# Kernel optimization log

Measured on AMD Instinct MI355X. Metric: run time of the kernel, lower is better.

Reference implementation:

```python
import jax, jax.numpy as jnp
import numpy as np

N, F_IN, E, DIM, G, C = 50000, 128, 800000, 64, 128, 10
BN_EPS = 1e-5


def setup_inputs() -> dict:
    key = jax.random.key(0)
    ks = jax.random.split(key, 24)
    x = jax.random.normal(ks[0], (N, F_IN), dtype=jnp.float32)
    edge_index = jax.random.randint(ks[1], (2, E), 0, N, dtype=jnp.int32)
    batch = jnp.sort(jax.random.randint(ks[2], (N,), 0, G, dtype=jnp.int32))

    def lin(k, fan_in, shape):
        b = 1.0 / np.sqrt(fan_in)
        return jax.random.uniform(k, shape, jnp.float32, -b, b)

    # layer 1 MLP: [F_IN->DIM], [DIM->DIM]
    W1a, b1a = lin(ks[3], F_IN, (F_IN, DIM)), lin(ks[4], F_IN, (DIM,))
    W1b, b1b = lin(ks[5], DIM, (DIM, DIM)), lin(ks[6], DIM, (DIM,))
    # layers 2-5 MLPs stacked: [4, DIM, DIM]
    Wa = jnp.stack([lin(jax.random.fold_in(ks[7], i), DIM, (DIM, DIM)) for i in range(4)])
    ba = jnp.stack([lin(jax.random.fold_in(ks[8], i), DIM, (DIM,)) for i in range(4)])
    Wb = jnp.stack([lin(jax.random.fold_in(ks[9], i), DIM, (DIM, DIM)) for i in range(4)])
    bb = jnp.stack([lin(jax.random.fold_in(ks[10], i), DIM, (DIM,)) for i in range(4)])
    gammas = jnp.ones((5, DIM), jnp.float32)
    betas = jnp.zeros((5, DIM), jnp.float32)
    fc1_w, fc1_b = lin(ks[11], DIM, (DIM, DIM)), lin(ks[12], DIM, (DIM,))
    fc2_w, fc2_b = lin(ks[13], DIM, (DIM, C)), lin(ks[14], DIM, (C,))
    return dict(x=x, edge_index=edge_index, batch=batch,
                W1a=W1a, b1a=b1a, W1b=W1b, b1b=b1b,
                Wa=Wa, ba=ba, Wb=Wb, bb=bb,
                gammas=gammas, betas=betas,
                fc1_w=fc1_w, fc1_b=fc1_b, fc2_w=fc2_w, fc2_b=fc2_b)


def _gin_conv(x, edge_index, W1, b1, W2, b2):
    # PyG GINConv (eps=0): MLP((1+eps)*x + scatter_add of source feats at targets)
    agg = jax.ops.segment_sum(x[edge_index[0]], edge_index[1], num_segments=N)
    h = x + agg
    h = jnp.maximum(h @ W1 + b1, 0.0) @ W2 + b2
    return h


def _bn(h, gamma, beta):
    # BatchNorm1d, training mode (batch statistics, biased variance)
    mean = h.mean(axis=0)
    var = h.var(axis=0)
    return (h - mean) * jax.lax.rsqrt(var + BN_EPS) * gamma + beta


def reference(x, edge_index, batch, W1a, b1a, W1b, b1b, Wa, ba, Wb, bb,
              gammas, betas, fc1_w, fc1_b, fc2_w, fc2_b):
    h = jnp.maximum(_gin_conv(x, edge_index, W1a, b1a, W1b, b1b), 0.0)
    h = _bn(h, gammas[0], betas[0])
    for i in range(4):
        h = jnp.maximum(_gin_conv(h, edge_index, Wa[i], ba[i], Wb[i], bb[i]), 0.0)
        h = _bn(h, gammas[i + 1], betas[i + 1])
    pooled = jax.ops.segment_sum(h, batch, num_segments=G)  # global_add_pool -> [G, DIM]
    z = jnp.maximum(pooled @ fc1_w + fc1_b, 0.0)
    z = z @ fc2_w + fc2_b
    return jax.nn.log_softmax(z, axis=-1)
```

## Files before the change

kernel.cpp:

```cpp
#include <hip/hip_runtime.h>
#include <hip/hip_fp16.h>


constexpr int N = 50000;
constexpr int E = 800000;
constexpr int G = 128;
constexpr int MAXDEG = 64;
constexpr int NPART = 8;
constexpr int PART_SZ = (N + NPART - 1) / NPART;
constexpr float BN_EPS = 1e-5f;

__device__ inline float4 ld4(const float* p) { return *(const float4*)p; }
__device__ inline void st4(float* p, float4 v) { *(float4*)p = v; }

union HF2 { __half2 h2[2]; float2 f2; };

__global__ __launch_bounds__(256) void count_fill_kernel(
    const int* __restrict__ ei, int* __restrict__ deg, unsigned short* __restrict__ ell)
{
    int part = blockIdx.x & (NPART - 1);
    int e = (blockIdx.x >> 3) * 256 + threadIdx.x;
    if (e < E) {
        int d = ei[E + e];
        if (d / PART_SZ == part) {
            int s = ei[e];
            int slot = atomicAdd(&deg[d], 1);
            if (slot < MAXDEG) ell[(size_t)d * MAXDEG + slot] = (unsigned short)s;
        }
    }
}

__global__ __launch_bounds__(256) void xw_kernel(
    const float* __restrict__ x, const float* __restrict__ W, __half* __restrict__ out)
{
    int tid = threadIdx.x;
    int ty = tid >> 4, tx = tid & 15;
    int base = blockIdx.x * 64;

    float acc[4][4];
#pragma unroll
    for (int r = 0; r < 4; r++)
#pragma unroll
        for (int cc = 0; cc < 4; cc++) acc[r][cc] = 0.f;

    int rr[4];
#pragma unroll
    for (int r = 0; r < 4; r++) rr[r] = min(base + 4 * ty + r, N - 1);

#pragma unroll 4
    for (int c = 0; c < 128; c++) {
        float4 w4 = ld4(W + c * 64 + 4 * tx);
#pragma unroll
        for (int r = 0; r < 4; r++) {
            float a = x[(size_t)rr[r] * 128 + c];
            acc[r][0] += a * w4.x; acc[r][1] += a * w4.y;
            acc[r][2] += a * w4.z; acc[r][3] += a * w4.w;
        }
    }
#pragma unroll
    for (int r = 0; r < 4; r++) {
        int node = base + 4 * ty + r;
        if (node < N) {
            HF2 u;
            u.h2[0] = __floats2half2_rn(acc[r][0], acc[r][1]);
            u.h2[1] = __floats2half2_rn(acc[r][2], acc[r][3]);
            *(float2*)(out + (size_t)node * 64 + 4 * tx) = u.f2;
        }
    }
}

__global__ __launch_bounds__(64) void reduce_stats_kernel(
    const float* __restrict__ partials, float* __restrict__ stats, int nb)
{
    int c = blockIdx.x;
    int lane = threadIdx.x;
    float s = 0.f;
    for (int i = lane; i < nb; i += 64)
        s += partials[(size_t)i * 128 + c];
#pragma unroll
    for (int off = 32; off > 0; off >>= 1)
        s += __shfl_down(s, off, 64);
    if (lane == 0) stats[c] = s;
}

template <bool FIRST>
__global__ __launch_bounds__(256) void layer_kernel(
    const __half* __restrict__ hin, const unsigned short* __restrict__ ell,
    const int* __restrict__ deg,
    const float* __restrict__ statsPrev, const float* __restrict__ gamma, const float* __restrict__ beta,
    const float* __restrict__ bias0,
    const float* __restrict__ W1, const float* __restrict__ b1,
    const float* __restrict__ W2, const float* __restrict__ b2,
    __half* __restrict__ hout, float* __restrict__ statsPart)
{
    __shared__ float sV[64 * 68];
    __shared__ float sStat[128];

    int tid = threadIdx.x, lane = tid & 63, wv = tid >> 6;
    if (tid < 128) sStat[tid] = 0.f;

    int base = blockIdx.x * 64;
    int n8 = lane >> 3, f = lane & 7;

    float sc[8], sh[8], b0[8];
    if constexpr (FIRST) {
#pragma unroll
        for (int q = 0; q < 2; q++) {
            float4 b4 = ld4(bias0 + 8 * f + 4 * q);
            b0[4 * q + 0] = b4.x; b0[4 * q + 1] = b4.y;
            b0[4 * q + 2] = b4.z; b0[4 * q + 3] = b4.w;
        }
    } else {
#pragma unroll
        for (int q = 0; q < 2; q++) {
            float4 s1 = ld4(statsPrev + 8 * f + 4 * q);
            float4 s2 = ld4(statsPrev + 64 + 8 * f + 4 * q);
            float4 g4 = ld4(gamma + 8 * f + 4 * q);
            float4 be4 = ld4(beta + 8 * f + 4 * q);
            float m[4] = { s1.x / N, s1.y / N, s1.z / N, s1.w / N };
            float v2[4] = { s2.x / N, s2.y / N, s2.z / N, s2.w / N };
            float gg[4] = { g4.x, g4.y, g4.z, g4.w };
            float bb4[4] = { be4.x, be4.y, be4.z, be4.w };
#pragma unroll
            for (int i = 0; i < 4; i++) {
                float s = gg[i] * rsqrtf(v2[i] - m[i] * m[i] + BN_EPS);
                sc[4 * q + i] = s;
                sh[4 * q + i] = bb4[i] - m[i] * s;
            }
        }
    }

    {
        int nodeA = base + wv * 16 + n8;
        int nodeB = nodeA + 8;
        int ndA = (nodeA < N) ? nodeA : N;
        int ndB = (nodeB < N) ? nodeB : N;
        int dgA = (nodeA < N) ? deg[nodeA] : 0;
        int dgB = (nodeB < N) ? deg[nodeB] : 0;
        int pA = (min(dgA, MAXDEG) + 7) & ~7;
        int pB = (min(dgB, MAXDEG) + 7) & ~7;
        int pm = max(pA, pB);
        const unsigned short* rowA = ell + (size_t)ndA * MAXDEG;
        const unsigned short* rowB = ell + (size_t)ndB * MAXDEG;

        __half2 apA[4][4], apB[4][4];
        __half2 z2 = __half2(__float2half(0.f), __float2half(0.f));
#pragma unroll
        for (int r = 0; r < 4; r++)
#pragma unroll
            for (int k = 0; k < 4; k++) { apA[r][k] = z2; apB[r][k] = z2; }

        float4 rownA = ld4((const float*)(hin + (size_t)ndA * 64 + 8 * f));
        float4 rownB = ld4((const float*)(hin + (size_t)ndB * 64 + 8 * f));

        for (int j = 0; j < pm; j += 8) {
            uint4 ivA = *(const uint4*)(rowA + j);
            uint4 ivB = *(const uint4*)(rowB + j);
            int a0 = min((int)(ivA.x & 0xFFFFu), N), a1 = min((int)(ivA.x >> 16), N);
            int a2 = min((int)(ivA.y & 0xFFFFu), N), a3 = min((int)(ivA.y >> 16), N);
            int a4 = min((int)(ivA.z & 0xFFFFu), N), a5 = min((int)(ivA.z >> 16), N);
            int a6 = min((int)(ivA.w & 0xFFFFu), N), a7 = min((int)(ivA.w >> 16), N);
            int b0i = min((int)(ivB.x & 0xFFFFu), N), b1i = min((int)(ivB.x >> 16), N);
            int b2i = min((int)(ivB.y & 0xFFFFu), N), b3i = min((int)(ivB.y >> 16), N);
            int b4i = min((int)(ivB.z & 0xFFFFu), N), b5i = min((int)(ivB.z >> 16), N);
            int b6i = min((int)(ivB.w & 0xFFFFu), N), b7i = min((int)(ivB.w >> 16), N);
            float4 rA0 = ld4((const float*)(hin + (size_t)a0 * 64 + 8 * f));
            float4 rA1 = ld4((const float*)(hin + (size_t)a1 * 64 + 8 * f));
            float4 rA2 = ld4((const float*)(hin + (size_t)a2 * 64 + 8 * f));
            float4 rA3 = ld4((const float*)(hin + (size_t)a3 * 64 + 8 * f));
            float4 rA4 = ld4((const float*)(hin + (size_t)a4 * 64 + 8 * f));
            float4 rA5 = ld4((const float*)(hin + (size_t)a5 * 64 + 8 * f));
            float4 rA6 = ld4((const float*)(hin + (size_t)a6 * 64 + 8 * f));
            float4 rA7 = ld4((const float*)(hin + (size_t)a7 * 64 + 8 * f));
            float4 rB0 = ld4((const float*)(hin + (size_t)b0i * 64 + 8 * f));
            float4 rB1 = ld4((const float*)(hin + (size_t)b1i * 64 + 8 * f));
            float4 rB2 = ld4((const float*)(hin + (size_t)b2i * 64 + 8 * f));
            float4 rB3 = ld4((const float*)(hin + (size_t)b3i * 64 + 8 * f));
            float4 rB4 = ld4((const float*)(hin + (size_t)b4i * 64 + 8 * f));
            float4 rB5 = ld4((const float*)(hin + (size_t)b5i * 64 + 8 * f));
            float4 rB6 = ld4((const float*)(hin + (size_t)b6i * 64 + 8 * f));
            float4 rB7 = ld4((const float*)(hin + (size_t)b7i * 64 + 8 * f));
            const __half2* hA0 = (const __half2*)&rA0; const __half2* hA1 = (const __half2*)&rA1;
            const __half2* hA2 = (const __half2*)&rA2; const __half2* hA3 = (const __half2*)&rA3;
            const __half2* hA4 = (const __half2*)&rA4; const __half2* hA5 = (const __half2*)&rA5;
            const __half2* hA6 = (const __half2*)&rA6; const __half2* hA7 = (const __half2*)&rA7;
            const __half2* hB0 = (const __half2*)&rB0; const __half2* hB1 = (const __half2*)&rB1;
            const __half2* hB2 = (const __half2*)&rB2; const __half2* hB3 = (const __half2*)&rB3;
            const __half2* hB4 = (const __half2*)&rB4; const __half2* hB5 = (const __half2*)&rB5;
            const __half2* hB6 = (const __half2*)&rB6; const __half2* hB7 = (const __half2*)&rB7;
#pragma unroll
            for (int k = 0; k < 4; k++) {
                apA[0][k] = __hadd2(apA[0][k], __hadd2(hA0[k], hA4[k]));
                apA[1][k] = __hadd2(apA[1][k], __hadd2(hA1[k], hA5[k]));
                apA[2][k] = __hadd2(apA[2][k], __hadd2(hA2[k], hA6[k]));
                apA[3][k] = __hadd2(apA[3][k], __hadd2(hA3[k], hA7[k]));
                apB[0][k] = __hadd2(apB[0][k], __hadd2(hB0[k], hB4[k]));
                apB[1][k] = __hadd2(apB[1][k], __hadd2(hB1[k], hB5[k]));
                apB[2][k] = __hadd2(apB[2][k], __hadd2(hB2[k], hB6[k]));
                apB[3][k] = __hadd2(apB[3][k], __hadd2(hB3[k], hB7[k]));
            }
        }

        const __half2* hoA = (const __half2*)&rownA;
        const __half2* hoB = (const __half2*)&rownB;
        float vA[8], vB[8];
#pragma unroll
        for (int k = 0; k < 4; k++) {
            float2 sA = __half22float2(hoA[k]);
            float2 sB = __half22float2(hoB[k]);
#pragma unroll
            for (int r = 0; r < 4; r++) {
                float2 fa = __half22float2(apA[r][k]);
                float2 fb = __half22float2(apB[r][k]);
                sA.x += fa.x; sA.y += fa.y;
                sB.x += fb.x; sB.y += fb.y;
            }
            if constexpr (FIRST) {
                vA[2 * k]     = fmaxf(sA.x + b0[2 * k], 0.f);
                vA[2 * k + 1] = fmaxf(sA.y + b0[2 * k + 1], 0.f);
                vB[2 * k]     = fmaxf(sB.x + b0[2 * k], 0.f);
                vB[2 * k + 1] = fmaxf(sB.y + b0[2 * k + 1], 0.f);
            } else {
                float dshA = (float)(1 + dgA);
                float dshB = (float)(1 + dgB);
                vA[2 * k]     = sc[2 * k] * sA.x + dshA * sh[2 * k];
                vA[2 * k + 1] = sc[2 * k + 1] * sA.y + dshA * sh[2 * k + 1];
                vB[2 * k]     = sc[2 * k] * sB.x + dshB * sh[2 * k];
                vB[2 * k + 1] = sc[2 * k + 1] * sB.y + dshB * sh[2 * k + 1];
            }
        }
        int ridxA = wv * 16 + n8;
        int ridxB = wv * 16 + 8 + n8;
        st4(sV + ridxA * 68 + 8 * f,     make_float4(vA[0], vA[1], vA[2], vA[3]));
        st4(sV + ridxA * 68 + 8 * f + 4, make_float4(vA[4], vA[5], vA[6], vA[7]));
        st4(sV + ridxB * 68 + 8 * f,     make_float4(vB[0], vB[1], vB[2], vB[3]));
        st4(sV + ridxB * 68 + 8 * f + 4, make_float4(vB[4], vB[5], vB[6], vB[7]));
    }
    __syncthreads();

    int ty = tid >> 4, tx = tid & 15;

    if constexpr (!FIRST) {
        float acc[4][4];
#pragma unroll
        for (int cc = 0; cc < 4; cc++) {
            float b = b1[4 * tx + cc];
            acc[0][cc] = b; acc[1][cc] = b; acc[2][cc] = b; acc[3][cc] = b;
        }
#pragma unroll 4
        for (int c = 0; c < 64; c++) {
            float4 w4 = ld4(W1 + c * 64 + 4 * tx);
#pragma unroll
            for (int r = 0; r < 4; r++) {
                float a = sV[(4 * ty + r) * 68 + c];
                acc[r][0] += a * w4.x; acc[r][1] += a * w4.y;
                acc[r][2] += a * w4.z; acc[r][3] += a * w4.w;
            }
        }
        __syncthreads();
#pragma unroll
        for (int r = 0; r < 4; r++)
            st4(sV + (4 * ty + r) * 68 + 4 * tx,
                make_float4(fmaxf(acc[r][0], 0.f), fmaxf(acc[r][1], 0.f),
                            fmaxf(acc[r][2], 0.f), fmaxf(acc[r][3], 0.f)));
        __syncthreads();
    }

    float acc[4][4];
#pragma unroll
    for (int cc = 0; cc < 4; cc++) {
        float b = b2[4 * tx + cc];
        acc[0][cc] = b; acc[1][cc] = b; acc[2][cc] = b; acc[3][cc] = b;
    }
#pragma unroll 4
    for (int c = 0; c < 64; c++) {
        float4 w4 = ld4(W2 + c * 64 + 4 * tx);
#pragma unroll
        for (int r = 0; r < 4; r++) {
            float a = sV[(4 * ty + r) * 68 + c];
            acc[r][0] += a * w4.x; acc[r][1] += a * w4.y;
            acc[r][2] += a * w4.z; acc[r][3] += a * w4.w;
        }
    }
#pragma unroll
    for (int r = 0; r < 4; r++) {
        int node = base + 4 * ty + r;
        if (node < N) {
            acc[r][0] = fmaxf(acc[r][0], 0.f); acc[r][1] = fmaxf(acc[r][1], 0.f);
            acc[r][2] = fmaxf(acc[r][2], 0.f); acc[r][3] = fmaxf(acc[r][3], 0.f);
            HF2 u;
            u.h2[0] = __floats2half2_rn(acc[r][0], acc[r][1]);
            u.h2[1] = __floats2half2_rn(acc[r][2], acc[r][3]);
            *(float2*)(hout + (size_t)node * 64 + 4 * tx) = u.f2;
        } else {
            acc[r][0] = acc[r][1] = acc[r][2] = acc[r][3] = 0.f;
        }
    }
#pragma unroll
    for (int cc = 0; cc < 4; cc++) {
        float s = 0.f, q = 0.f;
#pragma unroll
        for (int r = 0; r < 4; r++) { s += acc[r][cc]; q += acc[r][cc] * acc[r][cc]; }
        atomicAdd(&sStat[4 * tx + cc], s);
        atomicAdd(&sStat[64 + 4 * tx + cc], q);
    }
    __syncthreads();
    if (tid < 128) statsPart[(size_t)blockIdx.x * 128 + tid] = sStat[tid];
}

__global__ __launch_bounds__(256) void pool_head_kernel(
    const __half* __restrict__ h, const int* __restrict__ batch,
    const float* __restrict__ stats, const float* __restrict__ gamma, const float* __restrict__ beta,
    const float* __restrict__ fc1w, const float* __restrict__ fc1b,
    const float* __restrict__ fc2w, const float* __restrict__ fc2b,
    float* __restrict__ out)
{
    __shared__ float red[32][65];
    __shared__ float sp[64];
    __shared__ float sz[64];
    __shared__ float so[10];

    int tid = threadIdx.x;
    int g = blockIdx.x;

    int start, end;
    {
        int lo = 0, hi = N;
        while (lo < hi) { int mid = (lo + hi) >> 1; if (batch[mid] < g) lo = mid + 1; else hi = mid; }
        start = lo;
        lo = start; hi = N;
        while (lo < hi) { int mid = (lo + hi) >> 1; if (batch[mid] < g + 1) lo = mid + 1; else hi = mid; }
        end = lo;
    }

    int q = tid >> 3, sub = tid & 7;
    float a[8];
#pragma unroll
    for (int k = 0; k < 8; k++) a[k] = 0.f;

    for (int node = start + q; node < end; node += 32) {
        float4 raw = ld4((const float*)(h + (size_t)node * 64 + 8 * sub));
        const __half2* hh = (const __half2*)&raw;
#pragma unroll
        for (int k = 0; k < 4; k++) {
            float2 f2 = __half22float2(hh[k]);
            a[2 * k] += f2.x; a[2 * k + 1] += f2.y;
        }
    }
#pragma unroll
    for (int k = 0; k < 8; k++) red[q][8 * sub + k] = a[k];
    __syncthreads();

    if (tid < 64) {
        float t = 0.f;
#pragma unroll
        for (int qq = 0; qq < 32; qq++) t += red[qq][tid];
        float mean = stats[tid] * (1.f / N);
        float var  = stats[64 + tid] * (1.f / N) - mean * mean;
        float sc = gamma[tid] * rsqrtf(var + BN_EPS);
        float sh = beta[tid] - mean * sc;
        sp[tid] = sc * t + (float)(end - start) * sh;
    }
    __syncthreads();
    if (tid < 64) {
        float a1 = fc1b[tid];
#pragma unroll
        for (int c = 0; c < 64; c++) a1 += sp[c] * fc1w[c * 64 + tid];
        sz[tid] = fmaxf(a1, 0.f);
    }
    __syncthreads();
    if (tid < 10) {
        float z = fc2b[tid];
#pragma unroll
        for (int j = 0; j < 64; j++) z += sz[j] * fc2w[j * 10 + tid];
        so[tid] = z;
    }
    __syncthreads();
    if (tid < 10) {
        float m = -1e30f;
#pragma unroll
        for (int c = 0; c < 10; c++) m = fmaxf(m, so[c]);
        float s = 0.f;
#pragma unroll
        for (int c = 0; c < 10; c++) s += expf(so[c] - m);
        out[g * 10 + tid] = so[tid] - m - logf(s);
    }
}

extern "C" void kernel_launch(void* const* d_in, const int* in_sizes, int n_in,
                              void* d_out, int out_size, void* d_ws, size_t ws_size,
                              hipStream_t stream)
{
    const float* x    = (const float*)d_in[0];
    const int*   ei   = (const int*)  d_in[1];
    const int*   batch= (const int*)  d_in[2];
    const float* W1a  = (const float*)d_in[3];
    const float* b1a  = (const float*)d_in[4];
    const float* W1b  = (const float*)d_in[5];
    const float* b1b  = (const float*)d_in[6];
    const float* Wa   = (const float*)d_in[7];
    const float* ba   = (const float*)d_in[8];
    const float* Wb   = (const float*)d_in[9];
    const float* bb   = (const float*)d_in[10];
    const float* gammas = (const float*)d_in[11];
    const float* betas  = (const float*)d_in[12];
    const float* fc1w = (const float*)d_in[13];
    const float* fc1b = (const float*)d_in[14];
    const float* fc2w = (const float*)d_in[15];
    const float* fc2b = (const float*)d_in[16];
    float* out = (float*)d_out;

    char* w = (char*)d_ws;
    int*            deg      = (int*)w;
    float*          stats    = (float*)(w + 200704);
    unsigned short* ell      = (unsigned short*)(w + 203264);
    __half*         bufA     = (__half*)(w + 6603392);
    __half*         bufB     = (__half*)(w + 13003520);
    float*          partials = (float*)(w + 19403648);

    hipMemsetAsync(deg, 0, 200000, stream);
    hipMemsetAsync(ell, 0xFF, 6400128, stream);
    hipMemsetAsync(bufA + (size_t)N * 64, 0, 128, stream);
    hipMemsetAsync(bufB + (size_t)N * 64, 0, 128, stream);

    count_fill_kernel<<<NPART * ((E + 255) / 256), 256, 0, stream>>>(ei, deg, ell);
    xw_kernel<<<(N + 63) / 64, 256, 0, stream>>>(x, W1a, bufA);

    int nb = (N + 63) / 64;

    layer_kernel<true><<<nb, 256, 0, stream>>>(
        bufA, ell, deg, nullptr, nullptr, nullptr, b1a,
        nullptr, nullptr, W1b, b1b, bufB, partials);
    reduce_stats_kernel<<<128, 64, 0, stream>>>(partials, stats, nb);

    layer_kernel<false><<<nb, 256, 0, stream>>>(
        bufB, ell, deg, stats, gammas, betas, nullptr,
        Wa, ba, Wb, bb, bufA, partials);
    reduce_stats_kernel<<<128, 64, 0, stream>>>(partials, stats + 128, nb);

    layer_kernel<false><<<nb, 256, 0, stream>>>(
        bufA, ell, deg, stats + 128, gammas + 64, betas + 64, nullptr,
        Wa + 4096, ba + 64, Wb + 4096, bb + 64, bufB, partials);
    reduce_stats_kernel<<<128, 64, 0, stream>>>(partials, stats + 256, nb);

    layer_kernel<false><<<nb, 256, 0, stream>>>(
        bufB, ell, deg, stats + 256, gammas + 128, betas + 128, nullptr,
        Wa + 8192, ba + 128, Wb + 8192, bb + 128, bufA, partials);
    reduce_stats_kernel<<<128, 64, 0, stream>>>(partials, stats + 384, nb);

    layer_kernel<false><<<nb, 256, 0, stream>>>(
        bufA, ell, deg, stats + 384, gammas + 192, betas + 192, nullptr,
        Wa + 12288, ba + 192, Wb + 12288, bb + 192, bufB, partials);
    reduce_stats_kernel<<<128, 64, 0, stream>>>(partials, stats + 512, nb);

    pool_head_kernel<<<G, 256, 0, stream>>>(
        bufB, batch, stats + 512, gammas + 256, betas + 256,
        fc1w, fc1b, fc2w, fc2b, out);
}
```

Baseline: 418.2 us.

## Fuse graph build with first matmul and fold stats reduction into layer kernels

Merges the edge-bucketing kernel and the first-layer x@W kernel into one launch, with blocks split by index. Replaces the five separate BN-stats reduction kernels with a last-block-done ticket pattern: each layer block increments a counter, and the final block sums all partials and writes the stats. This removes six kernel launches and their gaps. In exchange, a single block now does the full serial reduction over about 782 partials, and the layer kernels depend on device-scope fences and counters that must be zeroed each call.

```diff
diff --git a/kernel.cpp b/kernel.cpp
--- a/kernel.cpp
+++ b/kernel.cpp
@@ -8,6 +8,8 @@
 constexpr int MAXDEG = 64;
 constexpr int NPART = 8;
 constexpr int PART_SZ = (N + NPART - 1) / NPART;
+constexpr int CF_BLOCKS = NPART * ((E + 255) / 256);
+constexpr int NB_TILES = (N + 63) / 64;
 constexpr float BN_EPS = 1e-5f;
 
 __device__ inline float4 ld4(const float* p) { return *(const float4*)p; }
@@ -15,27 +17,28 @@
 
 union HF2 { __half2 h2[2]; float2 f2; };
 
-__global__ __launch_bounds__(256) void count_fill_kernel(
-    const int* __restrict__ ei, int* __restrict__ deg, unsigned short* __restrict__ ell)
-{
-    int part = blockIdx.x & (NPART - 1);
-    int e = (blockIdx.x >> 3) * 256 + threadIdx.x;
-    if (e < E) {
-        int d = ei[E + e];
-        if (d / PART_SZ == part) {
-            int s = ei[e];
-            int slot = atomicAdd(&deg[d], 1);
-            if (slot < MAXDEG) ell[(size_t)d * MAXDEG + slot] = (unsigned short)s;
-        }
-    }
-}
-
-__global__ __launch_bounds__(256) void xw_kernel(
+__global__ __launch_bounds__(256) void build_kernel(
+    const int* __restrict__ ei, int* __restrict__ deg, unsigned short* __restrict__ ell,
     const float* __restrict__ x, const float* __restrict__ W, __half* __restrict__ out)
 {
     int tid = threadIdx.x;
+    if (blockIdx.x < CF_BLOCKS) {
+        int part = blockIdx.x & (NPART - 1);
+        int e = (blockIdx.x >> 3) * 256 + tid;
+        if (e < E) {
+            int d = ei[E + e];
+            if (d / PART_SZ == part) {
+                int s = ei[e];
+                int slot = atomicAdd(&deg[d], 1);
+                if (slot < MAXDEG) ell[(size_t)d * MAXDEG + slot] = (unsigned short)s;
+            }
+        }
+        return;
+    }
+
+    int tile = blockIdx.x - CF_BLOCKS;
     int ty = tid >> 4, tx = tid & 15;
-    int base = blockIdx.x * 64;
+    int base = tile * 64;
 
     float acc[4][4];
 #pragma unroll
@@ -67,20 +70,6 @@
             *(float2*)(out + (size_t)node * 64 + 4 * tx) = u.f2;
         }
     }
-}
-
-__global__ __launch_bounds__(64) void reduce_stats_kernel(
-    const float* __restrict__ partials, float* __restrict__ stats, int nb)
-{
-    int c = blockIdx.x;
-    int lane = threadIdx.x;
-    float s = 0.f;
-    for (int i = lane; i < nb; i += 64)
-        s += partials[(size_t)i * 128 + c];
-#pragma unroll
-    for (int off = 32; off > 0; off >>= 1)
-        s += __shfl_down(s, off, 64);
-    if (lane == 0) stats[c] = s;
 }
 
 template <bool FIRST>
@@ -91,10 +80,12 @@
     const float* __restrict__ bias0,
     const float* __restrict__ W1, const float* __restrict__ b1,
     const float* __restrict__ W2, const float* __restrict__ b2,
-    __half* __restrict__ hout, float* __restrict__ statsPart)
+    __half* __restrict__ hout, float* __restrict__ statsPart,
+    float* __restrict__ statsOut, int* __restrict__ doneCnt)
 {
     __shared__ float sV[64 * 68];
     __shared__ float sStat[128];
+    __shared__ int sTicket;
 
     int tid = threadIdx.x, lane = tid & 63, wv = tid >> 6;
     if (tid < 128) sStat[tid] = 0.f;
@@ -306,6 +297,19 @@
     }
     __syncthreads();
     if (tid < 128) statsPart[(size_t)blockIdx.x * 128 + tid] = sStat[tid];
+
+    __threadfence();
+    if (tid == 0) sTicket = atomicAdd(doneCnt, 1);
+    __syncthreads();
+    if (sTicket == (int)gridDim.x - 1) {
+        __threadfence();
+        if (tid < 128) {
+            float s = 0.f;
+            for (int i = 0; i < (int)gridDim.x; i++)
+                s += statsPart[(size_t)i * 128 + tid];
+            statsOut[tid] = s;
+        }
+    }
 }
 
 __global__ __launch_bounds__(256) void pool_head_kernel(
@@ -412,46 +416,39 @@
 
     char* w = (char*)d_ws;
     int*            deg      = (int*)w;
+    int*            doneCnt  = (int*)(w + 200000);
     float*          stats    = (float*)(w + 200704);
     unsigned short* ell      = (unsigned short*)(w + 203264);
     __half*         bufA     = (__half*)(w + 6603392);
     __half*         bufB     = (__half*)(w + 13003520);
     float*          partials = (float*)(w + 19403648);
 
-    hipMemsetAsync(deg, 0, 200000, stream);
+    hipMemsetAsync(deg, 0, 200020, stream);
     hipMemsetAsync(ell, 0xFF, 6400128, stream);
     hipMemsetAsync(bufA + (size_t)N * 64, 0, 128, stream);
     hipMemsetAsync(bufB + (size_t)N * 64, 0, 128, stream);
 
-    count_fill_kernel<<<NPART * ((E + 255) / 256), 256, 0, stream>>>(ei, deg, ell);
-    xw_kernel<<<(N + 63) / 64, 256, 0, stream>>>(x, W1a, bufA);
-
-    int nb = (N + 63) / 64;
-
-    layer_kernel<true><<<nb, 256, 0, stream>>>(
+    build_kernel<<<CF_BLOCKS + NB_TILES, 256, 0, stream>>>(ei, deg, ell, x, W1a, bufA);
+
+    layer_kernel<true><<<NB_TILES, 256, 0, stream>>>(
         bufA, ell, deg, nullptr, nullptr, nullptr, b1a,
-        nullptr, nullptr, W1b, b1b, bufB, partials);
-    reduce_stats_kernel<<<128, 64, 0, stream>>>(partials, stats, nb);
-
-    layer_kernel<false><<<nb, 256, 0, stream>>>(
+        nullptr, nullptr, W1b, b1b, bufB, partials, stats, doneCnt);
+
+    layer_kernel<false><<<NB_TILES, 256, 0, stream>>>(
         bufB, ell, deg, stats, gammas, betas, nullptr,
-        Wa, ba, Wb, bb, bufA, partials);
-    reduce_stats_kernel<<<128, 64, 0, stream>>>(partials, stats + 128, nb);
-
-    layer_kernel<false><<<nb, 256, 0, stream>>>(
+        Wa, ba, Wb, bb, bufA, partials, stats + 128, doneCnt + 1);
+
+    layer_kernel<false><<<NB_TILES, 256, 0, stream>>>(
         bufA, ell, deg, stats + 128, gammas + 64, betas + 64, nullptr,
-        Wa + 4096, ba + 64, Wb + 4096, bb + 64, bufB, partials);
-    reduce_stats_kernel<<<128, 64, 0, stream>>>(partials, stats + 256, nb);
-
-    layer_kernel<false><<<nb, 256, 0, stream>>>(
+        Wa + 4096, ba + 64, Wb + 4096, bb + 64, bufB, partials, stats + 256, doneCnt + 2);
+
+    layer_kernel<false><<<NB_TILES, 256, 0, stream>>>(
         bufB, ell, deg, stats + 256, gammas + 128, betas + 128, nullptr,
-        Wa + 8192, ba + 128, Wb + 8192, bb + 128, bufA, partials);
-    reduce_stats_kernel<<<128, 64, 0, stream>>>(partials, stats + 384, nb);
-
-    layer_kernel<false><<<nb, 256, 0, stream>>>(
+        Wa + 8192, ba + 128, Wb + 8192, bb + 128, bufA, partials, stats + 384, doneCnt + 3);
+
+    layer_kernel<false><<<NB_TILES, 256, 0, stream>>>(
         bufA, ell, deg, stats + 384, gammas + 192, betas + 192, nullptr,
-        Wa + 12288, ba + 192, Wb + 12288, bb + 192, bufB, partials);
-    reduce_stats_kernel<<<128, 64, 0, stream>>>(partials, stats + 512, nb);
+        Wa + 12288, ba + 192, Wb + 12288, bb + 192, bufB, partials, stats + 512, doneCnt + 4);
 
     pool_head_kernel<<<G, 256, 0, stream>>>(
         bufB, batch, stats + 512, gammas + 256, betas + 256,
```

Result: slower. 1.571 ms (+275.7%).
